# Kernel optimization log

Measured on AMD Instinct MI355X. Metric: run time of the kernel, lower is better.

The kernel has to match this reference:

```python
import jax, jax.numpy as jnp
import numpy as np

B, NPG, A, E = 128, 512, 8, 504   # graphs, nodes/graph, agents, edges/graph
F_IN, HID, H = 3, 64, 8
C = HID
F = H * C                          # 512 = concat head output
OUT = 2
NEG_SLOPE = 0.2


def _seg_softmax(alpha, dst, n):
    # edge-softmax normalized over destination-node neighborhoods
    m = jax.ops.segment_max(alpha, dst, num_segments=n)
    e = jnp.exp(alpha - m[dst])
    s = jax.ops.segment_sum(e, dst, num_segments=n)
    return e / jnp.clip(s[dst], 1e-16)


def _gat(x, src, dst, ea, W, b, a_s, a_d, We, a_e, n, self_loops):
    # PyG GATConv: heads=H, concat=True, edge_dim=1, fill_value='mean'
    xs = (x @ W).reshape(n, H, C)                      # [N,H,C]
    als = jnp.einsum('nhc,hc->nh', xs, a_s)            # alpha_src per node
    ald = jnp.einsum('nhc,hc->nh', xs, a_d)            # alpha_dst per node
    if self_loops:
        # fill_value='mean': self-loop attr = mean of incoming edge attrs
        ssum = jax.ops.segment_sum(ea, dst, num_segments=n)
        cnt = jax.ops.segment_sum(jnp.ones((dst.shape[0], 1), ea.dtype), dst, num_segments=n)
        loop_attr = ssum / jnp.maximum(cnt, 1.0)
        ea = jnp.concatenate([ea, loop_attr], axis=0)
        loop = jnp.arange(n, dtype=src.dtype)
        src = jnp.concatenate([src, loop])
        dst = jnp.concatenate([dst, loop])
    ee = (ea @ We).reshape(-1, H, C)                   # lin_edge
    ale = jnp.einsum('ehc,hc->eh', ee, a_e)            # alpha_edge per edge
    alpha = jax.nn.leaky_relu(als[src] + ald[dst] + ale, NEG_SLOPE)  # [E,H]
    alpha = _seg_softmax(alpha, dst, n)
    out = jax.ops.segment_sum(alpha[:, :, None] * xs[src], dst, num_segments=n)
    return out.reshape(n, H * C) + b


def _forward(x, edge_index, edge_attr, p1, p2, p3, fc1_w, fc1_b, fc2_w, fc2_b):
    Bq, npg, _ = x.shape
    n = Bq * npg
    off = (jnp.arange(Bq, dtype=edge_index.dtype) * npg)[:, None]   # PyG Batch offsets
    src = (edge_index[..., 0] + off).reshape(-1)
    dst = (edge_index[..., 1] + off).reshape(-1)
    ea = edge_attr.reshape(-1, 1)
    h = x.reshape(n, -1)
    h = jax.nn.relu(_gat(h, src, dst, ea, *p1, n, False))   # conv1: add_self_loops=False
    h = jax.nn.relu(_gat(h, src, dst, ea, *p2, n, True))
    h = jax.nn.relu(_gat(h, src, dst, ea, *p3, n, True))
    hg = h.reshape(Bq, npg, F)
    graph_emb = hg.mean(axis=1)                      # global_mean_pool (equal-size graphs)
    agent_emb = hg[:, :A].reshape(Bq * A, F)         # first num_agents nodes per graph
    comb = jnp.concatenate([agent_emb, jnp.repeat(graph_emb, A, axis=0)], axis=1)
    comb = jax.nn.relu(comb @ fc1_w + fc1_b)         # fc1 ReLU (extra torch.relu is idempotent)
    pred = comb @ fc2_w + fc2_b
    return pred.reshape(Bq, A, OUT)


def setup_inputs() -> dict:
    key = jax.random.key(0)
    ks = jax.random.split(key, 32)
    rn = lambda i, shape: jax.random.normal(ks[i], shape, jnp.float32) * 0.05
    inp = {
        'x': jax.random.normal(ks[0], (B, NPG, F_IN), jnp.float32),
        'edge_index': jax.random.randint(ks[1], (B, E, 2), 0, NPG, jnp.int32),
        'edge_attr': jax.random.normal(ks[2], (B, E, 1), jnp.float32),
    }
    dims = [F_IN, F, F]
    for li, din in enumerate(dims, start=1):
        inp[f'W{li}'] = rn(3 + li * 6, (din, H * C))
        inp[f'b{li}'] = jnp.zeros((H * C,), jnp.float32)
        inp[f'as{li}'] = rn(4 + li * 6, (H, C))
        inp[f'ad{li}'] = rn(5 + li * 6, (H, C))
        inp[f'We{li}'] = rn(6 + li * 6, (1, H * C))
        inp[f'ae{li}'] = rn(7 + li * 6, (H, C))
    inp['fc1_w'] = rn(28, (2 * F, 4 * HID))
    inp['fc1_b'] = jnp.zeros((4 * HID,), jnp.float32)
    inp['fc2_w'] = rn(29, (4 * HID, OUT))
    inp['fc2_b'] = jnp.zeros((OUT,), jnp.float32)
    return inp


def reference(x, edge_index, edge_attr,
              W1, b1, as1, ad1, We1, ae1,
              W2, b2, as2, ad2, We2, ae2,
              W3, b3, as3, ad3, We3, ae3,
              fc1_w, fc1_b, fc2_w, fc2_b):
    p1 = (W1, b1, as1, ad1, We1, ae1)
    p2 = (W2, b2, as2, ad2, We2, ae2)
    p3 = (W3, b3, as3, ad3, We3, ae3)
    return _forward(x, edge_index, edge_attr, p1, p2, p3, fc1_w, fc1_b, fc2_w, fc2_b)
```

## Files before the change

kernel.cpp:

```cpp
#include <hip/hip_runtime.h>
#include <hip/hip_bf16.h>
#include <math.h>

#define NGRAPH 128
#define NPG_   512
#define NN     (NGRAPH*NPG_)
#define EPG    504
#define ETOT   (NGRAPH*EPG)
#define HEADS  8
#define FDIM   512
#define NEG    0.2f

typedef __hip_bfloat16 bf16;
typedef __attribute__((ext_vector_type(8))) short short8;
typedef __attribute__((ext_vector_type(4))) float f32x4;

static __device__ __forceinline__ float bf(short s){
  union { unsigned u; float f; } c; c.u = ((unsigned)(unsigned short)s) << 16; return c.f;
}
static __device__ __forceinline__ short fbf(float v){
  bf16 b = __float2bfloat16(v); return *(short*)&b;
}

static __device__ __forceinline__ void gload16(void* lds, const void* g){
  __builtin_amdgcn_global_load_lds((const __attribute__((address_space(1))) void*)g,
                                   (__attribute__((address_space(3))) void*)lds, 16, 0, 0);
}

__global__ void k_sentinel(float* out, int n){
  int i = blockIdx.x*blockDim.x + threadIdx.x;
  if (i < n) out[i] = 12345.0f;
}

__global__ __launch_bounds__(512) void k_csr(const int* __restrict__ ei, const float* __restrict__ ea,
                                             const float* __restrict__ We0, const float* __restrict__ ae0,
                                             const float* __restrict__ We1, const float* __restrict__ ae1,
                                             const float* __restrict__ We2, const float* __restrict__ ae2,
                                             const float* __restrict__ W1,
                                             const float* __restrict__ as1, const float* __restrict__ ad1,
                                             int* __restrict__ deg_g, int* __restrict__ row_ptr,
                                             float* __restrict__ la,
                                             int* __restrict__ esrc, float* __restrict__ eattr,
                                             float* __restrict__ coef, float* __restrict__ wsd){
  int b = blockIdx.x;
  int t = threadIdx.x;
  if (b >= NGRAPH){
    if (b < NGRAPH+3){
      int l = b - NGRAPH;
      const float* We = l==0 ? We0 : (l==1 ? We1 : We2);
      const float* ae = l==0 ? ae0 : (l==1 ? ae1 : ae2);
      float v = We[t]*ae[t];
      #pragma unroll
      for (int o=32;o>0;o>>=1) v += __shfl_down(v, o);
      if ((t & 63) == 0) coef[l*HEADS + (t>>6)] = v;
      return;
    }
    float as_v = as1[t], ad_v = ad1[t];
    float v[6] = { W1[t]*as_v, W1[512+t]*as_v, W1[1024+t]*as_v,
                   W1[t]*ad_v, W1[512+t]*ad_v, W1[1024+t]*ad_v };
    #pragma unroll
    for (int o=32;o>0;o>>=1){
      #pragma unroll
      for (int q=0;q<6;q++) v[q] += __shfl_down(v[q], o);
    }
    if ((t & 63) == 0){
      int w = t >> 6;
      wsd[w*3+0]    = v[0]; wsd[w*3+1]    = v[1]; wsd[w*3+2]    = v[2];
      wsd[24+w*3+0] = v[3]; wsd[24+w*3+1] = v[4]; wsd[24+w*3+2] = v[5];
    }
    return;
  }
  __shared__ int   dg[512];
  __shared__ float ss[512];
  __shared__ int   scan[512];
  __shared__ int   cur[512];
  dg[t] = 0; ss[t] = 0.f;
  __syncthreads();
  int src=0, dst=0; float at=0.f;
  if (t < EPG){
    src = ei[(b*EPG+t)*2];
    dst = ei[(b*EPG+t)*2+1];
    at  = ea[b*EPG+t];
    atomicAdd(&dg[dst], 1);
    atomicAdd(&ss[dst], at);
  }
  __syncthreads();
  int d = dg[t];
  scan[t] = d;
  __syncthreads();
  for (int o=1;o<512;o<<=1){
    int v2 = (t>=o) ? scan[t-o] : 0;
    __syncthreads();
    scan[t] += v2;
    __syncthreads();
  }
  int excl = scan[t] - d;
  int n = b*NPG_ + t;
  row_ptr[n] = b*EPG + excl;
  deg_g[n]   = d;
  la[n]      = ss[t] / fmaxf((float)d, 1.f);
  cur[t] = excl;
  __syncthreads();
  if (t < EPG){
    int slot = atomicAdd(&cur[dst], 1);
    int p = b*EPG + slot;
    esrc[p]  = b*NPG_ + src;
    eattr[p] = at;
  }
}

__global__ void k_wt(const float* __restrict__ W1, const float* __restrict__ W2,
                     bf16* __restrict__ wt){
  int idx = blockIdx.x*blockDim.x + threadIdx.x;
  if (idx >= 2*FDIM*FDIM) return;
  int l = idx >> 18;
  int r = idx & (FDIM*FDIM-1);
  int n = r >> 9, k = r & 511;
  const float* W = l ? W2 : W1;
  wt[idx] = __float2bfloat16(W[k*FDIM + n]);
}

__global__ __launch_bounds__(256) void k_gat1(const float* __restrict__ x,
                                              const float* __restrict__ W,
                                              const float* __restrict__ wsd,
                                              const float* __restrict__ coef,
                                              const int* __restrict__ row_ptr,
                                              const int* __restrict__ deg,
                                              const int* __restrict__ esrc,
                                              const float* __restrict__ eattr,
                                              const float* __restrict__ bias,
                                              bf16* __restrict__ h){
  int nwg = gridDim.x;
  int cpx = nwg >> 3;
  int bid = blockIdx.x;
  int swz = (bid & 7)*cpx + (bid >> 3);
  int n = swz*4 + (threadIdx.x >> 6);
  int lane = threadIdx.x & 63;
  int hh = lane >> 3;
  int f0 = lane << 3;

  float ws0 = wsd[hh*3+0],    ws1 = wsd[hh*3+1],    ws2 = wsd[hh*3+2];
  float wd0 = wsd[24+hh*3+0], wd1 = wsd[24+hh*3+1], wd2 = wsd[24+hh*3+2];
  float ch = coef[hh];

  const float* xr = x + n*3;
  float aldn = xr[0]*wd0 + xr[1]*wd1 + xr[2]*wd2;

  int row = row_ptr[n], d = deg[n];
  float m = -1e30f, ssum = 0.f;
  float a0 = 0.f, a1 = 0.f, a2 = 0.f;
  for (int i=0;i<d;i++){
    int s = esrc[row+i]; float at = eattr[row+i];
    const float* xsr = x + s*3;
    float y0 = xsr[0], y1 = xsr[1], y2 = xsr[2];
    float raw = y0*ws0 + y1*ws1 + y2*ws2 + aldn + at*ch;
    raw = raw > 0.f ? raw : NEG*raw;
    float mn = fmaxf(m, raw);
    float sc = __expf(m - mn);
    float p  = __expf(raw - mn);
    ssum = ssum*sc + p;
    a0 = a0*sc + p*y0;
    a1 = a1*sc + p*y1;
    a2 = a2*sc + p*y2;
    m = mn;
  }
  float inv = 1.f / fmaxf(ssum, 1e-16f);
  a0 *= inv; a1 *= inv; a2 *= inv;

  float w0[8], w1[8], w2[8], b8[8];
  #pragma unroll
  for (int j=0;j<8;j+=4){
    *(float4*)&w0[j] = *(const float4*)&W[f0+j];
    *(float4*)&w1[j] = *(const float4*)&W[FDIM+f0+j];
    *(float4*)&w2[j] = *(const float4*)&W[2*FDIM+f0+j];
    *(float4*)&b8[j] = *(const float4*)&bias[f0+j];
  }
  short8 r;
  #pragma unroll
  for (int j=0;j<8;j++){
    float o = a0*w0[j] + a1*w1[j] + a2*w2[j] + b8[j];
    r[j] = fbf(o > 0.f ? o : 0.f);
  }
  ((short8*)(h + (size_t)n*FDIM))[lane] = r;
}

__global__ __launch_bounds__(256) void k_gat(const bf16* __restrict__ xs,
                                             const float* __restrict__ als,
                                             const float* __restrict__ ald,
                                             const float* __restrict__ coef,
                                             const int* __restrict__ row_ptr,
                                             const int* __restrict__ deg,
                                             const int* __restrict__ esrc,
                                             const float* __restrict__ eattr,
                                             const float* __restrict__ la,
                                             const float* __restrict__ bias,
                                             bf16* __restrict__ h){
  int nwg = gridDim.x;
  int cpx = nwg >> 3;
  int bid = blockIdx.x;
  int swz = (bid & 7)*cpx + (bid >> 3);
  int n = swz*4 + (threadIdx.x >> 6);
  int lane = threadIdx.x & 63;
  int hh = lane >> 3;
  int row = row_ptr[n], d = deg[n];
  int tot = d + 1;
  float aldn = ald[n*HEADS+hh];
  float ch = coef[hh];
  float lan = la[n];

  float m = -1e30f, ssum = 0.f;
  float acc[8] = {};
  for (int i=0;i<tot;i++){
    int s; float at;
    if (i<d){ s = esrc[row+i]; at = eattr[row+i]; }
    else    { s = n;           at = lan; }
    float raw = als[s*HEADS+hh] + aldn + at*ch;
    raw = raw > 0.f ? raw : NEG*raw;
    float mn = fmaxf(m, raw);
    float scale = __expf(m - mn);
    float p = __expf(raw - mn);
    ssum = ssum*scale + p;
    short8 v = ((const short8*)(xs + (size_t)s*FDIM))[lane];
    #pragma unroll
    for (int j=0;j<8;j++) acc[j] = acc[j]*scale + p*bf(v[j]);
    m = mn;
  }
  float inv = 1.f / fmaxf(ssum, 1e-16f);
  const float4* b4 = (const float4*)bias;
  float4 ba = b4[lane*2], bb = b4[lane*2+1];
  float bias8[8] = {ba.x,ba.y,ba.z,ba.w,bb.x,bb.y,bb.z,bb.w};
  short8 r;
  #pragma unroll
  for (int j=0;j<8;j++){
    float o = acc[j]*inv + bias8[j];
    r[j] = fbf(o > 0.f ? o : 0.f);
  }
  ((short8*)(h + (size_t)n*FDIM))[lane] = r;
}

__global__ __launch_bounds__(256) void gemm_mfma(const bf16* __restrict__ A,
                                                 const bf16* __restrict__ Wt,
                                                 const float* __restrict__ a_s,
                                                 const float* __restrict__ a_d,
                                                 bf16* __restrict__ C,
                                                 float* __restrict__ als,
                                                 float* __restrict__ ald,
                                                 int M, int N, int K){
  __shared__ short As[128*64];
  __shared__ short Bs[128*64];
  int bid = blockIdx.x;
  int wk = ((bid & 7) << 8) | (bid >> 3);
  const int bm = (wk >> 2)*128, bn = (wk & 3)*128;
  const int tid = threadIdx.x;
  const int lane = tid & 63;
  const int w = tid >> 6;
  const int wm = (w >> 1)*64, wn = (w & 1)*64;
  const int lr = lane & 15;
  const int lk = lane >> 4;

  f32x4 acc[4][4] = {};

  for (int k0 = 0; k0 < K; k0 += 64){
    #pragma unroll
    for (int is = 0; is < 4; ++is){
      int i = is*256 + tid;
      int r = i >> 3, g = i & 7;
      int gs = g ^ (r & 7);
      gload16(&As[i*8], A  + (size_t)(bm+r)*K + k0 + gs*8);
      gload16(&Bs[i*8], Wt + (size_t)(bn+r)*K + k0 + gs*8);
    }
    __syncthreads();
    #pragma unroll
    for (int kk = 0; kk < 2; ++kk){
      short8 af[4], bfr[4];
      #pragma unroll
      for (int mi=0; mi<4; ++mi){
        int row = wm + mi*16 + lr;
        int g = (kk*4 + lk) ^ (row & 7);
        af[mi] = *(const short8*)&As[row*64 + g*8];
      }
      #pragma unroll
      for (int ni=0; ni<4; ++ni){
        int row = wn + ni*16 + lr;
        int g = (kk*4 + lk) ^ (row & 7);
        bfr[ni] = *(const short8*)&Bs[row*64 + g*8];
      }
      #pragma unroll
      for (int mi=0; mi<4; ++mi)
        #pragma unroll
        for (int ni=0; ni<4; ++ni)
          acc[mi][ni] = __builtin_amdgcn_mfma_f32_16x16x32_bf16(af[mi], bfr[ni], acc[mi][ni], 0,0,0);
    }
    __syncthreads();
  }

  int hh = (bn + wn) >> 6;
  float as_c[4], ad_c[4];
  #pragma unroll
  for (int ni=0; ni<4; ++ni){
    int c = hh*64 + ni*16 + lr;
    as_c[ni] = a_s[c];
    ad_c[ni] = a_d[c];
  }
  #pragma unroll
  for (int mi=0; mi<4; ++mi)
    #pragma unroll
    for (int r=0; r<4; ++r){
      float s = acc[mi][0][r]*as_c[0] + acc[mi][1][r]*as_c[1]
              + acc[mi][2][r]*as_c[2] + acc[mi][3][r]*as_c[3];
      float d = acc[mi][0][r]*ad_c[0] + acc[mi][1][r]*ad_c[1]
              + acc[mi][2][r]*ad_c[2] + acc[mi][3][r]*ad_c[3];
      #pragma unroll
      for (int o=1;o<16;o<<=1){ s += __shfl_xor(s, o); d += __shfl_xor(d, o); }
      if (lr == 0){
        int rowg = bm + wm + mi*16 + lk*4 + r;
        als[rowg*HEADS+hh] = s;
        ald[rowg*HEADS+hh] = d;
      }
    }

  #pragma unroll
  for (int mi=0; mi<4; ++mi)
    #pragma unroll
    for (int ni=0; ni<4; ++ni){
      int col = bn + wn + ni*16 + lr;
      #pragma unroll
      for (int r=0; r<4; ++r){
        int rowg = bm + wm + mi*16 + lk*4 + r;
        C[(size_t)rowg*N + col] = __float2bfloat16(acc[mi][ni][r]);
      }
    }
}

__global__ __launch_bounds__(256) void k_gemb1(const bf16* __restrict__ h, float* __restrict__ pgemb){
  int gs_ = blockIdx.x;
  int g = gs_ >> 3, s = gs_ & 7;
  int t = threadIdx.x;
  int c = t & 63, rg = t >> 6;
  const bf16* base = h + ((size_t)(g*NPG_ + s*64 + rg*16))*FDIM;
  float acc[8] = {};
  #pragma unroll 4
  for (int i=0;i<16;i++){
    short8 v = ((const short8*)(base + (size_t)i*FDIM))[c];
    #pragma unroll
    for (int j=0;j<8;j++) acc[j] += bf(v[j]);
  }
  float* dst = pgemb + ((size_t)(gs_*4 + rg))*FDIM + c*8;
  float4 lo = {acc[0],acc[1],acc[2],acc[3]};
  float4 hi = {acc[4],acc[5],acc[6],acc[7]};
  *(float4*)dst = lo;
  *(float4*)(dst+4) = hi;
}

__global__ __launch_bounds__(256) void k_head1(const bf16* __restrict__ h,
                                               const float* __restrict__ pgemb,
                                               const float* __restrict__ fc1w,
                                               float* __restrict__ pf1,
                                               float* __restrict__ pge){
  __shared__ float ge[64];
  __shared__ float ag[8][64];
  int blk = blockIdx.x;
  int g = blk >> 3, q = blk & 7;
  int t = threadIdx.x;
  int k0 = q*64;

  if (t < 64){
    float s = 0.f;
    const float* p = pgemb + ((size_t)g*32)*FDIM + k0 + t;
    #pragma unroll 8
    for (int c=0;c<32;c++) s += p[(size_t)c*FDIM];
    ge[t] = s * (1.f/NPG_);
  } else if (t < 128){
    int i = t - 64;
    int r = i >> 3, c8 = i & 7;
    short8 v = ((const short8*)(h + ((size_t)(g*NPG_ + r))*FDIM + k0))[c8];
    #pragma unroll
    for (int j=0;j<8;j++) ag[r][c8*8+j] = bf(v[j]);
  }
  __syncthreads();

  float acc[8] = {};
  float gacc = 0.f;
  for (int kk=0; kk<64; kk++){
    float wa = fc1w[(size_t)(k0+kk)*256 + t];
    float wg = fc1w[(size_t)(FDIM+k0+kk)*256 + t];
    #pragma unroll
    for (int r=0;r<8;r++) acc[r] += ag[r][kk]*wa;
    gacc += ge[kk]*wg;
  }
  #pragma unroll
  for (int r=0;r<8;r++) pf1[((size_t)q*1024 + g*8 + r)*256 + t] = acc[r];
  pge[((size_t)q*NGRAPH + g)*256 + t] = gacc;
}

__global__ __launch_bounds__(256) void k_fc2(const float* __restrict__ pf1,
                                             const float* __restrict__ pge,
                                             const float* __restrict__ fc1b,
                                             const float* __restrict__ fc2w,
                                             const float* __restrict__ fc2b,
                                             float* __restrict__ out){
  __shared__ float f1[8][256];
  int g = blockIdx.x, t = threadIdx.x;
  float ges = 0.f;
  #pragma unroll
  for (int q=0;q<8;q++) ges += pge[((size_t)q*NGRAPH + g)*256 + t];
  float b = fc1b[t] + ges;
  #pragma unroll
  for (int r=0;r<8;r++){
    float s = 0.f;
    #pragma unroll
    for (int q=0;q<8;q++) s += pf1[((size_t)q*1024 + g*8 + r)*256 + t];
    f1[r][t] = fmaxf(s + b, 0.f);
  }
  __syncthreads();
  if (t < 128){
    int r = t >> 4, o = (t >> 3) & 1, l = t & 7;
    float s = 0.f;
    for (int k = l; k < 256; k += 8) s += f1[r][k] * fc2w[k*2+o];
    #pragma unroll
    for (int off=4; off; off>>=1) s += __shfl_down(s, off);
    if (l == 0) out[(g*8 + r)*2 + o] = s + fc2b[o];
  }
}

extern "C" void kernel_launch(void* const* d_in, const int* in_sizes, int n_in,
                              void* d_out, int out_size, void* d_ws, size_t ws_size,
                              hipStream_t stream)
{
  const float* x    = (const float*)d_in[0];
  const int*   ei   = (const int*)  d_in[1];
  const float* ea   = (const float*)d_in[2];
  const float* Wl[3]  = {(const float*)d_in[3],  (const float*)d_in[9],  (const float*)d_in[15]};
  const float* Bl[3]  = {(const float*)d_in[4],  (const float*)d_in[10], (const float*)d_in[16]};
  const float* ASl[3] = {(const float*)d_in[5],  (const float*)d_in[11], (const float*)d_in[17]};
  const float* ADl[3] = {(const float*)d_in[6],  (const float*)d_in[12], (const float*)d_in[18]};
  const float* WEl[3] = {(const float*)d_in[7],  (const float*)d_in[13], (const float*)d_in[19]};
  const float* AEl[3] = {(const float*)d_in[8],  (const float*)d_in[14], (const float*)d_in[20]};
  const float* FC1W = (const float*)d_in[21];
  const float* FC1B = (const float*)d_in[22];
  const float* FC2W = (const float*)d_in[23];
  const float* FC2B = (const float*)d_in[24];
  float* out = (float*)d_out;
  (void)in_sizes; (void)n_in;

  char* ws = (char*)d_ws;
  size_t off = 0;
  auto alloc = [&](size_t bytes)->char*{
    char* p = ws + off;
    off = (off + bytes + 255) & ~(size_t)255;
    return p;
  };
  bf16*  h       = (bf16*) alloc((size_t)NN*FDIM*2);
  bf16*  xs      = (bf16*) alloc((size_t)NN*FDIM*2);
  float* als     = (float*)alloc((size_t)NN*HEADS*4);
  float* ald     = (float*)alloc((size_t)NN*HEADS*4);
  float* la      = (float*)alloc((size_t)NN*4);
  int*   deg     = (int*)  alloc((size_t)NN*4);
  int*   row_ptr = (int*)  alloc((size_t)NN*4);
  int*   esrc    = (int*)  alloc((size_t)ETOT*4);
  float* eattr   = (float*)alloc((size_t)ETOT*4);
  float* coef    = (float*)alloc(3*HEADS*4);
  float* wsd     = (float*)alloc(48*4);
  bf16*  wt      = (bf16*) alloc((size_t)2*FDIM*FDIM*2);
  float* pgemb   = (float*)alloc((size_t)NGRAPH*32*FDIM*4);
  float* pf1     = (float*)alloc((size_t)8*1024*256*4);
  float* pge     = (float*)alloc((size_t)8*NGRAPH*256*4);

  if (off > ws_size){
    k_sentinel<<<(out_size+255)/256, 256, 0, stream>>>(out, out_size);
    return;
  }

  k_csr<<<NGRAPH+4, 512, 0, stream>>>(ei, ea, WEl[0], AEl[0], WEl[1], AEl[1], WEl[2], AEl[2],
                                      Wl[0], ASl[0], ADl[0],
                                      deg, row_ptr, la, esrc, eattr, coef, wsd);
  k_wt<<<(2*FDIM*FDIM+255)/256, 256, 0, stream>>>(Wl[1], Wl[2], wt);

  k_gat1<<<NN/4, 256, 0, stream>>>(x, Wl[0], wsd, coef, row_ptr, deg, esrc, eattr, Bl[0], h);

  for (int l=1;l<3;l++){
    gemm_mfma<<<2048, 256, 0, stream>>>(h, wt + (size_t)(l-1)*FDIM*FDIM,
                                        ASl[l], ADl[l], xs, als, ald, NN, FDIM, FDIM);
    k_gat<<<NN/4, 256, 0, stream>>>(xs, als, ald, coef + l*HEADS, row_ptr, deg, esrc, eattr, la, Bl[l], h);
  }

  k_gemb1<<<NGRAPH*8, 256, 0, stream>>>(h, pgemb);
  k_head1<<<NGRAPH*8, 256, 0, stream>>>(h, pgemb, FC1W, pf1, pge);
  k_fc2 <<<NGRAPH, 256, 0, stream>>>(pf1, pge, FC1B, FC2W, FC2B, out);
}
```

Before: 240.7 us.

## Stage GEMM output through swizzled LDS for coalesced stores; fuse weight transpose into CSR

The MFMA GEMM epilogue now writes the accumulator tile into a XOR-swizzled shared-memory buffer (reusing the A/B staging area), then stores full 16-byte rows to global memory instead of scattered 2-byte stores. Separately, the bf16 weight-transpose kernel is folded into the CSR build kernel as extra blocks, removing one launch. The cost is an extra LDS round trip and barrier in the GEMM epilogue, plus a larger grid for the CSR kernel.

```diff
diff --git a/kernel.cpp b/kernel.cpp
--- a/kernel.cpp
+++ b/kernel.cpp
@@ -38,10 +38,12 @@
                                              const float* __restrict__ We2, const float* __restrict__ ae2,
                                              const float* __restrict__ W1,
                                              const float* __restrict__ as1, const float* __restrict__ ad1,
+                                             const float* __restrict__ Wl2, const float* __restrict__ Wl3,
                                              int* __restrict__ deg_g, int* __restrict__ row_ptr,
                                              float* __restrict__ la,
                                              int* __restrict__ esrc, float* __restrict__ eattr,
-                                             float* __restrict__ coef, float* __restrict__ wsd){
+                                             float* __restrict__ coef, float* __restrict__ wsd,
+                                             bf16* __restrict__ wt){
   int b = blockIdx.x;
   int t = threadIdx.x;
   if (b >= NGRAPH){
@@ -55,19 +57,28 @@
       if ((t & 63) == 0) coef[l*HEADS + (t>>6)] = v;
       return;
     }
-    float as_v = as1[t], ad_v = ad1[t];
-    float v[6] = { W1[t]*as_v, W1[512+t]*as_v, W1[1024+t]*as_v,
-                   W1[t]*ad_v, W1[512+t]*ad_v, W1[1024+t]*ad_v };
-    #pragma unroll
-    for (int o=32;o>0;o>>=1){
-      #pragma unroll
-      for (int q=0;q<6;q++) v[q] += __shfl_down(v[q], o);
+    if (b == NGRAPH+3){
+      float as_v = as1[t], ad_v = ad1[t];
+      float v[6] = { W1[t]*as_v, W1[512+t]*as_v, W1[1024+t]*as_v,
+                     W1[t]*ad_v, W1[512+t]*ad_v, W1[1024+t]*ad_v };
+      #pragma unroll
+      for (int o=32;o>0;o>>=1){
+        #pragma unroll
+        for (int q=0;q<6;q++) v[q] += __shfl_down(v[q], o);
+      }
+      if ((t & 63) == 0){
+        int w = t >> 6;
+        wsd[w*3+0]    = v[0]; wsd[w*3+1]    = v[1]; wsd[w*3+2]    = v[2];
+        wsd[24+w*3+0] = v[3]; wsd[24+w*3+1] = v[4]; wsd[24+w*3+2] = v[5];
+      }
+      return;
     }
-    if ((t & 63) == 0){
-      int w = t >> 6;
-      wsd[w*3+0]    = v[0]; wsd[w*3+1]    = v[1]; wsd[w*3+2]    = v[2];
-      wsd[24+w*3+0] = v[3]; wsd[24+w*3+1] = v[4]; wsd[24+w*3+2] = v[5];
-    }
+    int idx = (b - (NGRAPH+4))*512 + t;
+    int l = idx >> 18;
+    int r = idx & (FDIM*FDIM-1);
+    int n = r >> 9, k = r & 511;
+    const float* W = l ? Wl3 : Wl2;
+    wt[idx] = __float2bfloat16(W[k*FDIM + n]);
     return;
   }
   __shared__ int   dg[512];
@@ -107,17 +118,6 @@
     esrc[p]  = b*NPG_ + src;
     eattr[p] = at;
   }
-}
-
-__global__ void k_wt(const float* __restrict__ W1, const float* __restrict__ W2,
-                     bf16* __restrict__ wt){
-  int idx = blockIdx.x*blockDim.x + threadIdx.x;
-  if (idx >= 2*FDIM*FDIM) return;
-  int l = idx >> 18;
-  int r = idx & (FDIM*FDIM-1);
-  int n = r >> 9, k = r & 511;
-  const float* W = l ? W2 : W1;
-  wt[idx] = __float2bfloat16(W[k*FDIM + n]);
 }
 
 __global__ __launch_bounds__(256) void k_gat1(const float* __restrict__ x,
@@ -246,8 +246,9 @@
                                                  float* __restrict__ als,
                                                  float* __restrict__ ald,
                                                  int M, int N, int K){
-  __shared__ short As[128*64];
-  __shared__ short Bs[128*64];
+  __shared__ short smem[128*128];
+  short* As = smem;
+  short* Bs = smem + 128*64;
   int bid = blockIdx.x;
   int wk = ((bid & 7) << 8) | (bid >> 3);
   const int bm = (wk >> 2)*128, bn = (wk & 3)*128;
@@ -319,17 +320,28 @@
       }
     }
 
+  short* Cs = smem;
   #pragma unroll
   for (int mi=0; mi<4; ++mi)
     #pragma unroll
     for (int ni=0; ni<4; ++ni){
-      int col = bn + wn + ni*16 + lr;
+      int col = wn + ni*16 + lr;
+      int g = col >> 3, c3 = col & 7;
       #pragma unroll
       for (int r=0; r<4; ++r){
-        int rowg = bm + wm + mi*16 + lk*4 + r;
-        C[(size_t)rowg*N + col] = __float2bfloat16(acc[mi][ni][r]);
+        int row = wm + mi*16 + lk*4 + r;
+        Cs[row*128 + ((g ^ (row & 15))<<3) + c3] = fbf(acc[mi][ni][r]);
       }
     }
+  __syncthreads();
+  #pragma unroll
+  for (int i2=0;i2<8;i2++){
+    int id = (i2<<8) + tid;
+    int row = id >> 4, seg = id & 15;
+    int gg = seg ^ (row & 15);
+    short8 v = *(const short8*)&Cs[row*128 + (gg<<3)];
+    ((short8*)(C + (size_t)(bm+row)*N + bn))[seg] = v;
+  }
 }
 
 __global__ __launch_bounds__(256) void k_gemb1(const bf16* __restrict__ h, float* __restrict__ pgemb){
@@ -471,10 +483,9 @@
     return;
   }
 
-  k_csr<<<NGRAPH+4, 512, 0, stream>>>(ei, ea, WEl[0], AEl[0], WEl[1], AEl[1], WEl[2], AEl[2],
-                                      Wl[0], ASl[0], ADl[0],
-                                      deg, row_ptr, la, esrc, eattr, coef, wsd);
-  k_wt<<<(2*FDIM*FDIM+255)/256, 256, 0, stream>>>(Wl[1], Wl[2], wt);
+  k_csr<<<NGRAPH+4+1024, 512, 0, stream>>>(ei, ea, WEl[0], AEl[0], WEl[1], AEl[1], WEl[2], AEl[2],
+                                           Wl[0], ASl[0], ADl[0], Wl[1], Wl[2],
+                                           deg, row_ptr, la, esrc, eattr, coef, wsd, wt);
 
   k_gat1<<<NN/4, 256, 0, stream>>>(x, Wl[0], wsd, coef, row_ptr, deg, esrc, eattr, Bl[0], h);
 
```

Measured after the change: 236.1 us. About the same (-1.9%).
